# Kernel tuning notes

Measured on AMD Instinct MI355X. Metric: run time of the kernel, lower is better.

The kernel has to match this reference:

```python
import jax, jax.numpy as jnp
import numpy as np

B, S, V = 2, 512, 151643
TEMP = 2.0
CE_W, KL_W = 1.0, 0.5


def setup_inputs() -> dict:
    key = jax.random.key(0)
    k1, k2, k3 = jax.random.split(key, 3)
    student_logits = jax.random.normal(k1, (B, S, V), dtype=jnp.float32)
    labels = jax.random.randint(k2, (B, S), 0, V, dtype=jnp.int32)
    attention_mask = jnp.ones((B, S), dtype=jnp.int32)
    # per-timestep teacher token logprobs (python floats in the original);
    # log of uniform gives realistic negative logprobs
    u = jax.random.uniform(k3, (S,), minval=1e-3, maxval=1.0, dtype=jnp.float32)
    teacher_token_logprobs = jnp.log(u)
    return dict(student_logits=student_logits,
                teacher_token_logprobs=teacher_token_logprobs,
                labels=labels,
                attention_mask=attention_mask)


def reference(student_logits, teacher_token_logprobs, labels, attention_mask):
    b, s, v = student_logits.shape
    dt = student_logits.dtype

    # ---- CE loss (F.cross_entropy, ignore_index=-100, mean over valid) ----
    logp = jax.nn.log_softmax(student_logits, axis=-1)          # [B,S,V]
    safe_labels = jnp.where(labels < 0, 0, labels)
    nll = -jnp.take_along_axis(logp, safe_labels[..., None], axis=-1)[..., 0]
    valid = (labels != -100)
    n_valid = jnp.maximum(valid.sum(), 1).astype(dt)
    ce_loss = jnp.sum(jnp.where(valid, nll, jnp.zeros((), dt))) / n_valid

    # ---- KL loss (kl_loss_from_logprobs) ----
    # teacher dist at step t is uniform with per-token prob p_t = (1-prob_t)/V,
    # so sum_v p_t*(log p_t - slp[b,t,v]) = V*p_t*log(p_t) - p_t * sum_v slp.
    slp = jax.nn.log_softmax(student_logits / TEMP, axis=-1)    # [B,S,V]
    slp_sum = slp.sum(axis=-1)                                  # [B,S]
    prob = jnp.minimum(jnp.exp(teacher_token_logprobs), 0.99)   # [S]
    p = (1.0 - prob) / v                                        # [S]
    kl_per_token = (v * p * jnp.log(p))[None, :] - p[None, :] * slp_sum  # [B,S]

    mask = attention_mask[:, :s].astype(dt)
    masked = (kl_per_token * mask).sum()
    num_valid = mask.sum()
    kl_loss = jnp.where(num_valid > 0, masked / num_valid, masked) * (TEMP ** 2)

    total = CE_W * ce_loss + KL_W * kl_loss
    return total
```

## Files before the change

### kernel.cpp

```cpp
#include <hip/hip_runtime.h>
#include <math.h>

constexpr int B = 2, S = 512, V = 151643;
constexpr int NROWS = B * S;
constexpr float TEMP = 2.0f;
constexpr float CE_W = 1.0f, KL_W = 0.5f;
constexpr int BLK = 256;
constexpr int V4 = V >> 2;
constexpr int MAIN4 = (V4 / (2 * BLK)) * (2 * BLK);

__global__ __launch_bounds__(BLK) void row_stats_kernel(
    const float* __restrict__ logits,
    const int*   __restrict__ labels,
    float* __restrict__ nll_out,
    float* __restrict__ slpsum_out)
{
    const int row = blockIdx.x;
    const float* __restrict__ x = logits + (size_t)row * V;
    const int tid = threadIdx.x;
    const float4* __restrict__ x4 = reinterpret_cast<const float4*>(x);

    float m = -INFINITY, mthr = -INFINITY;
    float sA[4], tA[4], uA[4], sB[4], tB[4], uB[4];
    #pragma unroll
    for (int j = 0; j < 4; ++j) {
        sA[j] = tA[j] = uA[j] = 0.f;
        sB[j] = tB[j] = uB[j] = 0.f;
    }

    auto upd = [&](float xv, float& sS, float& tS, float& uS) {
        uS += xv;
        if (xv > mthr) {
            float r  = __expf((m - xv) * 0.5f);
            float r2 = r * r;
            #pragma unroll
            for (int j = 0; j < 4; ++j) {
                tA[j] *= r;  sA[j] *= r2;
                tB[j] *= r;  sB[j] *= r2;
            }
            m = xv; mthr = xv + 8.0f;
        }
        float e = __expf((xv - m) * 0.5f);
        tS += e;
        sS = fmaf(e, e, sS);
    };

    for (int i = tid; i < MAIN4; i += 2 * BLK) {
        float4 a = x4[i];
        float4 b = x4[i + BLK];
        upd(a.x, sA[0], tA[0], uA[0]);
        upd(a.y, sA[1], tA[1], uA[1]);
        upd(a.z, sA[2], tA[2], uA[2]);
        upd(a.w, sA[3], tA[3], uA[3]);
        upd(b.x, sB[0], tB[0], uB[0]);
        upd(b.y, sB[1], tB[1], uB[1]);
        upd(b.z, sB[2], tB[2], uB[2]);
        upd(b.w, sB[3], tB[3], uB[3]);
    }
    if (MAIN4 + tid < V4) {
        float4 a = x4[MAIN4 + tid];
        upd(a.x, sA[0], tA[0], uA[0]);
        upd(a.y, sA[1], tA[1], uA[1]);
        upd(a.z, sA[2], tA[2], uA[2]);
        upd(a.w, sA[3], tA[3], uA[3]);
    }
    if ((V4 << 2) + tid < V) {
        upd(x[(V4 << 2) + tid], sA[0], tA[0], uA[0]);
    }

    float s = 0.f, sT = 0.f, sumx = 0.f;
    #pragma unroll
    for (int j = 0; j < 4; ++j) {
        s    += sA[j] + sB[j];
        sT   += tA[j] + tB[j];
        sumx += uA[j] + uB[j];
    }

    #pragma unroll
    for (int off = 32; off >= 1; off >>= 1) {
        float m2  = __shfl_xor(m,    off, 64);
        float s2  = __shfl_xor(s,    off, 64);
        float sT2 = __shfl_xor(sT,   off, 64);
        float sx2 = __shfl_xor(sumx, off, 64);
        float nm = fmaxf(m, m2);
        float e1 = __expf((m - nm) * 0.5f), e2 = __expf((m2 - nm) * 0.5f);
        s  = s  * (e1 * e1) + s2 * (e2 * e2);
        sT = sT * e1 + sT2 * e2;
        m  = nm;
        sumx += sx2;
    }

    __shared__ float red[4][4];
    const int wave = tid >> 6, lane = tid & 63;
    if (lane == 0) {
        red[wave][0] = m; red[wave][1] = s; red[wave][2] = sT; red[wave][3] = sumx;
    }
    __syncthreads();
    if (tid == 0) {
        m = red[0][0]; s = red[0][1]; sT = red[0][2]; sumx = red[0][3];
        #pragma unroll
        for (int w = 1; w < 4; ++w) {
            float m2 = red[w][0], s2 = red[w][1], sT2 = red[w][2];
            float nm = fmaxf(m, m2);
            float e1 = __expf((m - nm) * 0.5f), e2 = __expf((m2 - nm) * 0.5f);
            s  = s  * (e1 * e1) + s2 * (e2 * e2);
            sT = sT * e1 + sT2 * e2;
            m  = nm;
            sumx += red[w][3];
        }
        const float logZ = m + logf(s);
        const int lab  = labels[row];
        const int safe = lab < 0 ? 0 : lab;
        nll_out[row] = logZ - x[safe];
        const float logZT = m * (1.0f / TEMP) + logf(sT);
        slpsum_out[row] = sumx * (1.0f / TEMP) - (float)V * logZT;
    }
}

__global__ __launch_bounds__(1024) void finalize_kernel(
    const float* __restrict__ nll,
    const float* __restrict__ slpsum,
    const int*   __restrict__ labels,
    const int*   __restrict__ amask,
    const float* __restrict__ tlp,
    float* __restrict__ out)
{
    const int t = threadIdx.x;
    const int srow = t % S;

    const int lab = labels[t];
    const bool valid = (lab != -100);
    float ce_n = valid ? nll[t] : 0.f;
    float ce_d = valid ? 1.f : 0.f;

    const float prob = fminf(expf(tlp[srow]), 0.99f);
    const float p = (1.0f - prob) / (float)V;
    const float kl = ((float)V * p * logf(p)) - p * slpsum[t];
    const float msk = (float)amask[t];
    float kl_n = kl * msk;
    float kl_d = msk;

    #pragma unroll
    for (int off = 32; off >= 1; off >>= 1) {
        ce_n += __shfl_xor(ce_n, off, 64);
        ce_d += __shfl_xor(ce_d, off, 64);
        kl_n += __shfl_xor(kl_n, off, 64);
        kl_d += __shfl_xor(kl_d, off, 64);
    }

    __shared__ float red[16][4];
    const int wave = t >> 6, lane = t & 63;
    if (lane == 0) {
        red[wave][0] = ce_n; red[wave][1] = ce_d;
        red[wave][2] = kl_n; red[wave][3] = kl_d;
    }
    __syncthreads();
    if (t == 0) {
        float a = 0.f, b = 0.f, c = 0.f, d = 0.f;
        #pragma unroll
        for (int w = 0; w < 16; ++w) {
            a += red[w][0]; b += red[w][1]; c += red[w][2]; d += red[w][3];
        }
        const float ce  = a / fmaxf(b, 1.0f);
        const float klv = (d > 0.f ? c / d : c) * (TEMP * TEMP);
        out[0] = CE_W * ce + KL_W * klv;
    }
}

extern "C" void kernel_launch(void* const* d_in, const int* in_sizes, int n_in,
                              void* d_out, int out_size, void* d_ws, size_t ws_size,
                              hipStream_t stream) {
    const float* logits = (const float*)d_in[0];
    const float* tlp    = (const float*)d_in[1];
    const int*   labels = (const int*)d_in[2];
    const int*   amask  = (const int*)d_in[3];
    float* out = (float*)d_out;

    float* nll    = (float*)d_ws;
    float* slpsum = nll + NROWS;

    row_stats_kernel<<<NROWS, BLK, 0, stream>>>(logits, labels, nll, slpsum);
    finalize_kernel<<<1, 1024, 0, stream>>>(nll, slpsum, labels, amask, tlp, out);
}
```

Before: 114.6 us.

## Split each row across two blocks and merge partial softmax stats in finalize

Measured after the change: 124.0 us. +8.2%, slower.

```diff
diff --git a/kernel.cpp b/kernel.cpp
--- a/kernel.cpp
+++ b/kernel.cpp
@@ -7,18 +7,18 @@
 constexpr float CE_W = 1.0f, KL_W = 0.5f;
 constexpr int BLK = 256;
 constexpr int V4 = V >> 2;
-constexpr int MAIN4 = (V4 / (2 * BLK)) * (2 * BLK);
+constexpr int H4 = V4 / 2;
+constexpr int HMAIN4 = (H4 / (2 * BLK)) * (2 * BLK);
 
-__global__ __launch_bounds__(BLK) void row_stats_kernel(
+__global__ __launch_bounds__(BLK) void row_stats_partial(
     const float* __restrict__ logits,
-    const int*   __restrict__ labels,
-    float* __restrict__ nll_out,
-    float* __restrict__ slpsum_out)
+    float4* __restrict__ partials)
 {
-    const int row = blockIdx.x;
+    const int g = blockIdx.x;
+    const int row = g >> 1, half = g & 1;
     const float* __restrict__ x = logits + (size_t)row * V;
+    const float4* __restrict__ x4 = reinterpret_cast<const float4*>(x) + half * H4;
     const int tid = threadIdx.x;
-    const float4* __restrict__ x4 = reinterpret_cast<const float4*>(x);
 
     float m = -INFINITY, mthr = -INFINITY;
     float sA[4], tA[4], uA[4], sB[4], tB[4], uB[4];
@@ -45,7 +45,7 @@
         sS = fmaf(e, e, sS);
     };
 
-    for (int i = tid; i < MAIN4; i += 2 * BLK) {
+    for (int i = tid; i < HMAIN4; i += 2 * BLK) {
         float4 a = x4[i];
         float4 b = x4[i + BLK];
         upd(a.x, sA[0], tA[0], uA[0]);
@@ -57,14 +57,14 @@
         upd(b.z, sB[2], tB[2], uB[2]);
         upd(b.w, sB[3], tB[3], uB[3]);
     }
-    if (MAIN4 + tid < V4) {
-        float4 a = x4[MAIN4 + tid];
+    if (HMAIN4 + tid < H4) {
+        float4 a = x4[HMAIN4 + tid];
         upd(a.x, sA[0], tA[0], uA[0]);
         upd(a.y, sA[1], tA[1], uA[1]);
         upd(a.z, sA[2], tA[2], uA[2]);
         upd(a.w, sA[3], tA[3], uA[3]);
     }
-    if ((V4 << 2) + tid < V) {
+    if (half == 1 && tid < V - (V4 << 2)) {
         upd(x[(V4 << 2) + tid], sA[0], tA[0], uA[0]);
     }
 
@@ -108,18 +108,13 @@
             m  = nm;
             sumx += red[w][3];
         }
-        const float logZ = m + logf(s);
-        const int lab  = labels[row];
-        const int safe = lab < 0 ? 0 : lab;
-        nll_out[row] = logZ - x[safe];
-        const float logZT = m * (1.0f / TEMP) + logf(sT);
-        slpsum_out[row] = sumx * (1.0f / TEMP) - (float)V * logZT;
+        partials[g] = make_float4(m, s, sT, sumx);
     }
 }
 
 __global__ __launch_bounds__(1024) void finalize_kernel(
-    const float* __restrict__ nll,
-    const float* __restrict__ slpsum,
+    const float4* __restrict__ partials,
+    const float* __restrict__ logits,
     const int*   __restrict__ labels,
     const int*   __restrict__ amask,
     const float* __restrict__ tlp,
@@ -128,14 +123,31 @@
     const int t = threadIdx.x;
     const int srow = t % S;
 
+    const float4 pa = partials[2 * t];
+    const float4 pb = partials[2 * t + 1];
+    const float nm = fmaxf(pa.x, pb.x);
+    const float e1 = __expf((pa.x - nm) * 0.5f);
+    const float e2 = __expf((pb.x - nm) * 0.5f);
+    const float s    = pa.y * (e1 * e1) + pb.y * (e2 * e2);
+    const float sT   = pa.z * e1 + pb.z * e2;
+    const float sumx = pa.w + pb.w;
+
     const int lab = labels[t];
+    const int safe = lab < 0 ? 0 : lab;
+    const float xl = logits[(size_t)t * V + safe];
+
+    const float logZ = nm + logf(s);
+    const float nllv = logZ - xl;
+    const float logZT = nm * (1.0f / TEMP) + logf(sT);
+    const float slpsum = sumx * (1.0f / TEMP) - (float)V * logZT;
+
     const bool valid = (lab != -100);
-    float ce_n = valid ? nll[t] : 0.f;
+    float ce_n = valid ? nllv : 0.f;
     float ce_d = valid ? 1.f : 0.f;
 
     const float prob = fminf(expf(tlp[srow]), 0.99f);
     const float p = (1.0f - prob) / (float)V;
-    const float kl = ((float)V * p * logf(p)) - p * slpsum[t];
+    const float kl = ((float)V * p * logf(p)) - p * slpsum;
     const float msk = (float)amask[t];
     float kl_n = kl * msk;
     float kl_d = msk;
@@ -176,9 +188,8 @@
     const int*   amask  = (const int*)d_in[3];
     float* out = (float*)d_out;
 
-    float* nll    = (float*)d_ws;
-    float* slpsum = nll + NROWS;
+    float4* partials = (float4*)d_ws;
 
-    row_stats_kernel<<<NROWS, BLK, 0, stream>>>(logits, labels, nll, slpsum);
-    finalize_kernel<<<1, 1024, 0, stream>>>(nll, slpsum, labels, amask, tlp, out);
+    row_stats_partial<<<2 * NROWS, BLK, 0, stream>>>(logits, partials);
+    finalize_kernel<<<1, 1024, 0, stream>>>(partials, logits, labels, amask, tlp, out);
 }
```

## Fuse finalize into row kernel with atomics and align row float4 loads

Applied to the files above, without the earlier changes.

After: 179.4 us. 56.6% more time.

```diff
diff --git a/kernel.cpp b/kernel.cpp
--- a/kernel.cpp
+++ b/kernel.cpp
@@ -6,19 +6,33 @@
 constexpr float TEMP = 2.0f;
 constexpr float CE_W = 1.0f, KL_W = 0.5f;
 constexpr int BLK = 256;
-constexpr int V4 = V >> 2;
-constexpr int MAIN4 = (V4 / (2 * BLK)) * (2 * BLK);
+constexpr int N4 = 37910;
+constexpr int MAIN4 = (N4 / (2 * BLK)) * (2 * BLK);
 
-__global__ __launch_bounds__(BLK) void row_stats_kernel(
+__global__ __launch_bounds__(BLK) void fused_kernel(
     const float* __restrict__ logits,
     const int*   __restrict__ labels,
-    float* __restrict__ nll_out,
-    float* __restrict__ slpsum_out)
+    const int*   __restrict__ amask,
+    const float* __restrict__ tlp,
+    float* __restrict__ accs,
+    float* __restrict__ out)
 {
     const int row = blockIdx.x;
     const float* __restrict__ x = logits + (size_t)row * V;
     const int tid = threadIdx.x;
-    const float4* __restrict__ x4 = reinterpret_cast<const float4*>(x);
+
+    const int off  = (int)((uintptr_t)x & 15);
+    const int head = ((16 - off) & 15) >> 2;
+    const float* __restrict__ xa = x + head;
+    const float4* __restrict__ xa4 = reinterpret_cast<const float4*>(xa);
+
+    int lab = 0; float xl = 0.f, tlpv = 0.f; int mskI = 0;
+    if (tid == 0) {
+        lab  = labels[row];
+        xl   = x[lab < 0 ? 0 : lab];
+        tlpv = tlp[row & (S - 1)];
+        mskI = amask[row];
+    }
 
     float m = -INFINITY, mthr = -INFINITY;
     float sA[4], tA[4], uA[4], sB[4], tB[4], uB[4];
@@ -45,9 +59,11 @@
         sS = fmaf(e, e, sS);
     };
 
+    if (tid < head) upd(x[tid], sB[0], tB[0], uB[0]);
+
     for (int i = tid; i < MAIN4; i += 2 * BLK) {
-        float4 a = x4[i];
-        float4 b = x4[i + BLK];
+        float4 a = xa4[i];
+        float4 b = xa4[i + BLK];
         upd(a.x, sA[0], tA[0], uA[0]);
         upd(a.y, sA[1], tA[1], uA[1]);
         upd(a.z, sA[2], tA[2], uA[2]);
@@ -57,15 +73,15 @@
         upd(b.z, sB[2], tB[2], uB[2]);
         upd(b.w, sB[3], tB[3], uB[3]);
     }
-    if (MAIN4 + tid < V4) {
-        float4 a = x4[MAIN4 + tid];
+    if (MAIN4 + tid < N4) {
+        float4 a = xa4[MAIN4 + tid];
         upd(a.x, sA[0], tA[0], uA[0]);
         upd(a.y, sA[1], tA[1], uA[1]);
         upd(a.z, sA[2], tA[2], uA[2]);
         upd(a.w, sA[3], tA[3], uA[3]);
     }
-    if ((V4 << 2) + tid < V) {
-        upd(x[(V4 << 2) + tid], sA[0], tA[0], uA[0]);
+    if (tid < 3 - head) {
+        upd(xa[4 * N4 + tid], sA[0], tA[0], uA[0]);
     }
 
     float s = 0.f, sT = 0.f, sumx = 0.f;
@@ -77,11 +93,11 @@
     }
 
     #pragma unroll
-    for (int off = 32; off >= 1; off >>= 1) {
-        float m2  = __shfl_xor(m,    off, 64);
-        float s2  = __shfl_xor(s,    off, 64);
-        float sT2 = __shfl_xor(sT,   off, 64);
-        float sx2 = __shfl_xor(sumx, off, 64);
+    for (int offx = 32; offx >= 1; offx >>= 1) {
+        float m2  = __shfl_xor(m,    offx, 64);
+        float s2  = __shfl_xor(s,    offx, 64);
+        float sT2 = __shfl_xor(sT,   offx, 64);
+        float sx2 = __shfl_xor(sumx, offx, 64);
         float nm = fmaxf(m, m2);
         float e1 = __expf((m - nm) * 0.5f), e2 = __expf((m2 - nm) * 0.5f);
         s  = s  * (e1 * e1) + s2 * (e2 * e2);
@@ -108,62 +124,33 @@
             m  = nm;
             sumx += red[w][3];
         }
-        const float logZ = m + logf(s);
-        const int lab  = labels[row];
-        const int safe = lab < 0 ? 0 : lab;
-        nll_out[row] = logZ - x[safe];
+        const float logZ  = m + logf(s);
+        const float nllv  = logZ - xl;
         const float logZT = m * (1.0f / TEMP) + logf(sT);
-        slpsum_out[row] = sumx * (1.0f / TEMP) - (float)V * logZT;
-    }
-}
+        const float slpsum = sumx * (1.0f / TEMP) - (float)V * logZT;
 
-__global__ __launch_bounds__(1024) void finalize_kernel(
-    const float* __restrict__ nll,
-    const float* __restrict__ slpsum,
-    const int*   __restrict__ labels,
-    const int*   __restrict__ amask,
-    const float* __restrict__ tlp,
-    float* __restrict__ out)
-{
-    const int t = threadIdx.x;
-    const int srow = t % S;
+        const bool valid = (lab != -100);
+        const float prob = fminf(expf(tlpv), 0.99f);
+        const float p = (1.0f - prob) / (float)V;
+        const float kl = ((float)V * p * logf(p)) - p * slpsum;
+        const float msk = (float)mskI;
 
-    const int lab = labels[t];
-    const bool valid = (lab != -100);
-    float ce_n = valid ? nll[t] : 0.f;
-    float ce_d = valid ? 1.f : 0.f;
-
-    const float prob = fminf(expf(tlp[srow]), 0.99f);
-    const float p = (1.0f - prob) / (float)V;
-    const float kl = ((float)V * p * logf(p)) - p * slpsum[t];
-    const float msk = (float)amask[t];
-    float kl_n = kl * msk;
-    float kl_d = msk;
-
-    #pragma unroll
-    for (int off = 32; off >= 1; off >>= 1) {
-        ce_n += __shfl_xor(ce_n, off, 64);
-        ce_d += __shfl_xor(ce_d, off, 64);
-        kl_n += __shfl_xor(kl_n, off, 64);
-        kl_d += __shfl_xor(kl_d, off, 64);
-    }
-
-    __shared__ float red[16][4];
-    const int wave = t >> 6, lane = t & 63;
-    if (lane == 0) {
-        red[wave][0] = ce_n; red[wave][1] = ce_d;
-        red[wave][2] = kl_n; red[wave][3] = kl_d;
-    }
-    __syncthreads();
-    if (t == 0) {
-        float a = 0.f, b = 0.f, c = 0.f, d = 0.f;
-        #pragma unroll
-        for (int w = 0; w < 16; ++w) {
-            a += red[w][0]; b += red[w][1]; c += red[w][2]; d += red[w][3];
+        atomicAdd(&accs[0], valid ? nllv : 0.f);
+        atomicAdd(&accs[1], valid ? 1.f : 0.f);
+        atomicAdd(&accs[2], kl * msk);
+        atomicAdd(&accs[3], msk);
+        __threadfence();
+        unsigned old = atomicAdd(reinterpret_cast<unsigned*>(&accs[4]), 1u);
+        if (old == (unsigned)(NROWS - 1)) {
+            __threadfence();
+            float a = __hip_atomic_load(&accs[0], __ATOMIC_RELAXED, __HIP_MEMORY_SCOPE_AGENT);
+            float b = __hip_atomic_load(&accs[1], __ATOMIC_RELAXED, __HIP_MEMORY_SCOPE_AGENT);
+            float c = __hip_atomic_load(&accs[2], __ATOMIC_RELAXED, __HIP_MEMORY_SCOPE_AGENT);
+            float d = __hip_atomic_load(&accs[3], __ATOMIC_RELAXED, __HIP_MEMORY_SCOPE_AGENT);
+            const float ce  = a / fmaxf(b, 1.0f);
+            const float klv = (d > 0.f ? c / d : c) * (TEMP * TEMP);
+            out[0] = CE_W * ce + KL_W * klv;
         }
-        const float ce  = a / fmaxf(b, 1.0f);
-        const float klv = (d > 0.f ? c / d : c) * (TEMP * TEMP);
-        out[0] = CE_W * ce + KL_W * klv;
     }
 }
 
@@ -174,11 +161,9 @@
     const float* tlp    = (const float*)d_in[1];
     const int*   labels = (const int*)d_in[2];
     const int*   amask  = (const int*)d_in[3];
-    float* out = (float*)d_out;
+    float* out  = (float*)d_out;
+    float* accs = (float*)d_ws;
 
-    float* nll    = (float*)d_ws;
-    float* slpsum = nll + NROWS;
-
-    row_stats_kernel<<<NROWS, BLK, 0, stream>>>(logits, labels, nll, slpsum);
-    finalize_kernel<<<1, 1024, 0, stream>>>(nll, slpsum, labels, amask, tlp, out);
+    hipMemsetAsync(accs, 0, 5 * sizeof(float), stream);
+    fused_kernel<<<NROWS, BLK, 0, stream>>>(logits, labels, amask, tlp, accs, out);
 }
```
